# Kernel tuning notes

Hardware: AMD Instinct MI355X
Metric: run time of the kernel (lower is better)

The kernel has to match this reference:

```python
import jax, jax.numpy as jnp
import numpy as np
import math

B, S, D, H = 2, 2048, 1024, 16
DK = D // H


def setup_inputs() -> dict:
    key = jax.random.key(0)
    k1, k2, k3, k4, k5 = jax.random.split(key, 5)
    x = jax.random.normal(k1, (B, S, D), dtype=jnp.float32)
    # causal mask: True above the diagonal (positions to 'mask').
    causal_mask = jnp.triu(jnp.ones((S, S), dtype=bool), k=1)[None, None, :, :]
    scale = 1.0 / math.sqrt(D)
    W_qkv = jax.random.normal(k2, (D, 3 * D), dtype=jnp.float32) * scale
    b_qkv = jax.random.normal(k3, (3 * D,), dtype=jnp.float32) * 0.01
    W_out = jax.random.normal(k4, (D, D), dtype=jnp.float32) * scale
    b_out = jax.random.normal(k5, (D,), dtype=jnp.float32) * 0.01
    return {"x": x, "causal_mask": causal_mask, "W_qkv": W_qkv,
            "b_qkv": b_qkv, "W_out": W_out, "b_out": b_out}


def reference(x, causal_mask, W_qkv, b_qkv, W_out, b_out):
    b, s, d = x.shape
    qkv = x @ W_qkv + b_qkv                       # [b, s, 3d]
    q, k, v = jnp.split(qkv, 3, axis=-1)
    def heads(t):  # [b, s, d] -> [b, h, s, dk]
        return t.reshape(b, s, H, DK).transpose(0, 2, 1, 3)
    q, k, v = heads(q), heads(k), heads(v)
    scores = jnp.einsum("bhqd,bhkd->bhqk", q, k) / math.sqrt(DK)
    # Faithful to original: masked_fill_(mask, 1e9) uses POSITIVE 1e9.
    scores = jnp.where(causal_mask, jnp.float32(1e9), scores)
    attn = jax.nn.softmax(scores, axis=-1)        # [b, h, s, s]
    out = jnp.einsum("bhqk,bhkd->bhqd", attn, v)  # [b, h, s, dk]
    out = out.transpose(0, 2, 1, 3).reshape(b, s, d)
    return out @ W_out + b_out
```

## Files before the change

### kernel.cpp

```cpp
#include <hip/hip_runtime.h>
#include <hip/hip_bf16.h>
#include <cstdint>

constexpr int SEQ = 2048;
constexpr int DIM = 1024;
constexpr int NH = 16;
constexpr int DKH = 64;
constexpr int TRIPLE = 3072;
constexpr int BS = 2;
constexpr int MROWS = BS * SEQ;

typedef __bf16 bf16x8 __attribute__((ext_vector_type(8)));
typedef __bf16 bf16x4 __attribute__((ext_vector_type(4)));
typedef float f32x4 __attribute__((ext_vector_type(4)));

__global__ void cast_f32_bf16(const float* __restrict__ in, __bf16* __restrict__ out, int n4) {
  int i = blockIdx.x * blockDim.x + threadIdx.x;
  if (i < n4) {
    float4 v = reinterpret_cast<const float4*>(in)[i];
    bf16x4 o;
    o[0] = (__bf16)v.x; o[1] = (__bf16)v.y; o[2] = (__bf16)v.z; o[3] = (__bf16)v.w;
    reinterpret_cast<bf16x4*>(out)[i] = o;
  }
}

__global__ void transpose_cast(const float* __restrict__ W, __bf16* __restrict__ Wt,
                               int K, int N) {
  __shared__ float t[32][33];
  int c0 = blockIdx.x * 32;
  int r0 = blockIdx.y * 32;
  int tx = threadIdx.x, ty = threadIdx.y;
#pragma unroll
  for (int i = 0; i < 4; i++)
    t[ty + i * 8][tx] = W[(size_t)(r0 + ty + i * 8) * N + c0 + tx];
  __syncthreads();
#pragma unroll
  for (int i = 0; i < 4; i++)
    Wt[(size_t)(c0 + ty + i * 8) * K + r0 + tx] = (__bf16)t[tx][ty + i * 8];
}

__device__ __forceinline__ void async_copy16(const void* g, void* l) {
  __builtin_amdgcn_global_load_lds(
      (const __attribute__((address_space(1))) unsigned int*)g,
      (__attribute__((address_space(3))) unsigned int*)l, 16, 0, 0);
}

template <bool OUT_BF16>
__global__ void gemm_bt(const __bf16* __restrict__ A, const __bf16* __restrict__ Bt,
                        const float* __restrict__ bias, void* __restrict__ Cv,
                        int M, int N, int K) {
  constexpr int BM = 128, BN = 128, BK = 32;
  __shared__ __align__(16) __bf16 As[BM][BK];
  __shared__ __align__(16) __bf16 Bs[BN][BK];
  const int tid = threadIdx.x;
  const int lane = tid & 63;
  const int wave = tid >> 6;
  const int bm = blockIdx.x * BM;
  const int bn = blockIdx.y * BN;
  const int wr = (wave >> 1) * 64;
  const int wc = (wave & 1) * 64;

  f32x4 acc[4][4] = {};

  const int r15 = lane & 15;
  const int kq = (lane >> 4) * 8;

  for (int k0 = 0; k0 < K; k0 += BK) {
#pragma unroll
    for (int j = 0; j < 2; j++) {
      int seg = j * 256 + tid;
      int row = seg >> 2;
      int col = (seg & 3) * 8;
      const __bf16* ga = A + (size_t)(bm + row) * K + k0 + col;
      char* la = (char*)(&As[0][0]) + (size_t)(j * 256 + (tid & 192)) * 16;
      async_copy16(ga, la);
      const __bf16* gb = Bt + (size_t)(bn + row) * K + k0 + col;
      char* lb = (char*)(&Bs[0][0]) + (size_t)(j * 256 + (tid & 192)) * 16;
      async_copy16(gb, lb);
    }
    __syncthreads();

    bf16x8 af[4], bfr[4];
#pragma unroll
    for (int i = 0; i < 4; i++)
      af[i] = *reinterpret_cast<const bf16x8*>(&As[wr + i * 16 + r15][kq]);
#pragma unroll
    for (int j = 0; j < 4; j++)
      bfr[j] = *reinterpret_cast<const bf16x8*>(&Bs[wc + j * 16 + r15][kq]);
#pragma unroll
    for (int i = 0; i < 4; i++)
#pragma unroll
      for (int j = 0; j < 4; j++)
        acc[i][j] = __builtin_amdgcn_mfma_f32_16x16x32_bf16(af[i], bfr[j], acc[i][j], 0, 0, 0);
    __syncthreads();
  }

  __bf16* Cb = (__bf16*)Cv;
  float* Cf = (float*)Cv;
#pragma unroll
  for (int i = 0; i < 4; i++) {
    int row0 = bm + wr + i * 16 + ((lane >> 4) << 2);
#pragma unroll
    for (int j = 0; j < 4; j++) {
      int col = bn + wc + j * 16 + (lane & 15);
      float bv = bias[col];
#pragma unroll
      for (int jj = 0; jj < 4; jj++) {
        float v = acc[i][j][jj] + bv;
        if constexpr (OUT_BF16)
          Cb[(size_t)(row0 + jj) * N + col] = (__bf16)v;
        else
          Cf[(size_t)(row0 + jj) * N + col] = v;
      }
    }
  }
}

__global__ __launch_bounds__(64) void chunk_sums_k(const __bf16* __restrict__ qkv,
                                                   float* __restrict__ cs) {
  int bh = blockIdx.x, c = blockIdx.y, dk = threadIdx.x;
  int b = bh >> 4, h = bh & 15;
  const __bf16* vbase = qkv + (size_t)b * SEQ * TRIPLE + 2 * DIM + h * DKH + dk;
  float acc = 0.f;
#pragma unroll 8
  for (int kk = 0; kk < 64; kk++)
    acc += (float)vbase[(size_t)(c * 64 + kk) * TRIPLE];
  cs[((bh * 32 + c) << 6) + dk] = acc;
}

__global__ __launch_bounds__(64) void suffix_mean_k(const __bf16* __restrict__ qkv,
                                                    const float* __restrict__ cs,
                                                    __bf16* __restrict__ attn) {
  int bh = blockIdx.x, c = blockIdx.y, dk = threadIdx.x;
  int b = bh >> 4, h = bh & 15;
  float acc = 0.f;
  for (int c2 = c + 1; c2 < 32; c2++) acc += cs[((bh * 32 + c2) << 6) + dk];
  const __bf16* vbase = qkv + (size_t)b * SEQ * TRIPLE + 2 * DIM + h * DKH + dk;
  __bf16* obase = attn + (size_t)b * SEQ * DIM + h * DKH + dk;
#pragma unroll 8
  for (int kk = 63; kk >= 0; kk--) {
    int q = c * 64 + kk;
    if (q != SEQ - 1)
      obase[(size_t)q * DIM] = (__bf16)(acc / (float)(SEQ - 1 - q));
    acc += (float)vbase[(size_t)q * TRIPLE];
  }
}

__global__ __launch_bounds__(256) void last_row_attn(const __bf16* __restrict__ qkv,
                                                     __bf16* __restrict__ attn) {
  const int bh = blockIdx.x, b = bh >> 4, h = bh & 15;
  const int tid = threadIdx.x;
  __shared__ float qv[64];
  __shared__ float p[SEQ];
  __shared__ float red[4];
  __shared__ float red2[4];
  __shared__ float part[4][64];
  const __bf16* base = qkv + (size_t)b * SEQ * TRIPLE;
  if (tid < 64) qv[tid] = (float)base[(size_t)(SEQ - 1) * TRIPLE + h * DKH + tid];
  __syncthreads();
  float ls[8];
  float lmax = -1e30f;
#pragma unroll
  for (int i = 0; i < 8; i++) {
    int k = tid + i * 256;
    const bf16x8* kp = reinterpret_cast<const bf16x8*>(base + (size_t)k * TRIPLE + DIM + h * DKH);
    float dot = 0.f;
#pragma unroll
    for (int u = 0; u < 8; u++) {
      bf16x8 kv = kp[u];
#pragma unroll
      for (int e = 0; e < 8; e++) dot += qv[u * 8 + e] * (float)kv[e];
    }
    ls[i] = dot * 0.125f;
    lmax = fmaxf(lmax, ls[i]);
  }
#pragma unroll
  for (int off = 32; off >= 1; off >>= 1) lmax = fmaxf(lmax, __shfl_xor(lmax, off));
  if ((tid & 63) == 0) red[tid >> 6] = lmax;
  __syncthreads();
  lmax = fmaxf(fmaxf(red[0], red[1]), fmaxf(red[2], red[3]));
  float lsum = 0.f;
#pragma unroll
  for (int i = 0; i < 8; i++) {
    float e = expf(ls[i] - lmax);
    p[tid + i * 256] = e;
    lsum += e;
  }
#pragma unroll
  for (int off = 32; off >= 1; off >>= 1) lsum += __shfl_xor(lsum, off);
  if ((tid & 63) == 0) red2[tid >> 6] = lsum;
  __syncthreads();
  float Z = red2[0] + red2[1] + red2[2] + red2[3];
  int dk = tid & 63, ch = tid >> 6;
  float acc = 0.f;
  const __bf16* vb = base + 2 * DIM + h * DKH + dk;
  for (int k = ch * 512; k < (ch + 1) * 512; k++) acc += p[k] * (float)vb[(size_t)k * TRIPLE];
  part[ch][dk] = acc;
  __syncthreads();
  if (tid < 64) {
    float s = (part[0][tid] + part[1][tid] + part[2][tid] + part[3][tid]) / Z;
    attn[((size_t)b * SEQ + (SEQ - 1)) * DIM + h * DKH + tid] = (__bf16)s;
  }
}

extern "C" void kernel_launch(void* const* d_in, const int* in_sizes, int n_in,
                              void* d_out, int out_size, void* d_ws, size_t ws_size,
                              hipStream_t stream) {
  const float* x = (const float*)d_in[0];
  const float* Wqkv = (const float*)d_in[2];
  const float* bqkv = (const float*)d_in[3];
  const float* Wout = (const float*)d_in[4];
  const float* bout = (const float*)d_in[5];
  float* out = (float*)d_out;

  char* ws = (char*)d_ws;
  __bf16* xb = (__bf16*)ws;
  __bf16* wqkvT = (__bf16*)(ws + (8u << 20));
  __bf16* woutT = (__bf16*)(ws + (14u << 20));
  __bf16* qkvb = (__bf16*)(ws + (16u << 20));
  __bf16* attnb = (__bf16*)(ws + (40u << 20));
  float* csums = (float*)(ws + (48u << 20));

  cast_f32_bf16<<<(MROWS * DIM / 4 + 255) / 256, 256, 0, stream>>>(x, xb, MROWS * DIM / 4);
  transpose_cast<<<dim3(TRIPLE / 32, DIM / 32), dim3(32, 8), 0, stream>>>(Wqkv, wqkvT, DIM, TRIPLE);
  transpose_cast<<<dim3(DIM / 32, DIM / 32), dim3(32, 8), 0, stream>>>(Wout, woutT, DIM, DIM);

  gemm_bt<true><<<dim3(MROWS / 128, TRIPLE / 128), 256, 0, stream>>>(
      xb, wqkvT, bqkv, (void*)qkvb, MROWS, TRIPLE, DIM);

  chunk_sums_k<<<dim3(BS * NH, 32), 64, 0, stream>>>(qkvb, csums);
  suffix_mean_k<<<dim3(BS * NH, 32), 64, 0, stream>>>(qkvb, csums, attnb);
  last_row_attn<<<BS * NH, 256, 0, stream>>>(qkvb, attnb);

  gemm_bt<false><<<dim3(MROWS / 128, DIM / 128), 256, 0, stream>>>(
      attnb, woutT, bout, (void*)out, MROWS, DIM, DIM);
}
```

Measured before the change: 205.7 us.

## Skip Q projection except last row; split last-row attention across chunks

The QKV GEMM now computes only the K and V columns. The single query row still needed (the last position, the only row not fully masked) is computed by a small dot-product kernel. The last-row attention is split into 32 chunk-parallel partial softmax blocks plus a combine kernel, replacing one 256-thread block per head that ran serially over 2048 keys. This removes a third of the projection GEMM work and raises parallelism on the last-row tail, at the cost of two extra launches.

```diff
diff --git a/kernel.cpp b/kernel.cpp
--- a/kernel.cpp
+++ b/kernel.cpp
@@ -7,6 +7,7 @@
 constexpr int NH = 16;
 constexpr int DKH = 64;
 constexpr int TRIPLE = 3072;
+constexpr int KVSTR = 2048;
 constexpr int BS = 2;
 constexpr int MROWS = BS * SEQ;
 
@@ -116,91 +117,111 @@
   }
 }
 
-__global__ __launch_bounds__(64) void chunk_sums_k(const __bf16* __restrict__ qkv,
+__global__ __launch_bounds__(64) void qlast_k(const __bf16* __restrict__ xb,
+                                              const __bf16* __restrict__ wqkvT,
+                                              const float* __restrict__ bqkv,
+                                              float* __restrict__ qlast) {
+  int b = blockIdx.x;
+  int col = blockIdx.y * 64 + threadIdx.x;
+  const __bf16* xrow = xb + ((size_t)(b * SEQ + SEQ - 1)) * DIM;
+  const __bf16* wrow = wqkvT + (size_t)col * DIM;
+  float acc = 0.f;
+#pragma unroll 8
+  for (int u = 0; u < DIM / 8; u++) {
+    bf16x8 a = reinterpret_cast<const bf16x8*>(xrow)[u];
+    bf16x8 w = reinterpret_cast<const bf16x8*>(wrow)[u];
+#pragma unroll
+    for (int e = 0; e < 8; e++) acc += (float)a[e] * (float)w[e];
+  }
+  qlast[b * DIM + col] = acc + bqkv[col];
+}
+
+__global__ __launch_bounds__(64) void chunk_sums_k(const __bf16* __restrict__ kv,
                                                    float* __restrict__ cs) {
   int bh = blockIdx.x, c = blockIdx.y, dk = threadIdx.x;
   int b = bh >> 4, h = bh & 15;
-  const __bf16* vbase = qkv + (size_t)b * SEQ * TRIPLE + 2 * DIM + h * DKH + dk;
+  const __bf16* vbase = kv + (size_t)b * SEQ * KVSTR + DIM + h * DKH + dk;
   float acc = 0.f;
 #pragma unroll 8
   for (int kk = 0; kk < 64; kk++)
-    acc += (float)vbase[(size_t)(c * 64 + kk) * TRIPLE];
+    acc += (float)vbase[(size_t)(c * 64 + kk) * KVSTR];
   cs[((bh * 32 + c) << 6) + dk] = acc;
 }
 
-__global__ __launch_bounds__(64) void suffix_mean_k(const __bf16* __restrict__ qkv,
+__global__ __launch_bounds__(64) void suffix_mean_k(const __bf16* __restrict__ kv,
                                                     const float* __restrict__ cs,
                                                     __bf16* __restrict__ attn) {
   int bh = blockIdx.x, c = blockIdx.y, dk = threadIdx.x;
   int b = bh >> 4, h = bh & 15;
   float acc = 0.f;
   for (int c2 = c + 1; c2 < 32; c2++) acc += cs[((bh * 32 + c2) << 6) + dk];
-  const __bf16* vbase = qkv + (size_t)b * SEQ * TRIPLE + 2 * DIM + h * DKH + dk;
+  const __bf16* vbase = kv + (size_t)b * SEQ * KVSTR + DIM + h * DKH + dk;
   __bf16* obase = attn + (size_t)b * SEQ * DIM + h * DKH + dk;
 #pragma unroll 8
   for (int kk = 63; kk >= 0; kk--) {
     int q = c * 64 + kk;
     if (q != SEQ - 1)
       obase[(size_t)q * DIM] = (__bf16)(acc / (float)(SEQ - 1 - q));
-    acc += (float)vbase[(size_t)q * TRIPLE];
-  }
-}
-
-__global__ __launch_bounds__(256) void last_row_attn(const __bf16* __restrict__ qkv,
-                                                     __bf16* __restrict__ attn) {
+    acc += (float)vbase[(size_t)q * KVSTR];
+  }
+}
+
+__global__ __launch_bounds__(64) void lastrow_partial(const __bf16* __restrict__ kv,
+                                                      const float* __restrict__ qlast,
+                                                      float* __restrict__ pm,
+                                                      float* __restrict__ pz,
+                                                      float* __restrict__ pwv) {
+  const int bh = blockIdx.x, c = blockIdx.y;
+  const int b = bh >> 4, h = bh & 15;
+  const int t = threadIdx.x;
+  __shared__ float qs[64];
+  __shared__ float pe[64];
+  qs[t] = qlast[b * DIM + h * DKH + t];
+  __syncthreads();
+  const __bf16* krow = kv + ((size_t)(b * SEQ + c * 64 + t)) * KVSTR + h * DKH;
+  float dot = 0.f;
+#pragma unroll
+  for (int u = 0; u < 8; u++) {
+    bf16x8 kw = reinterpret_cast<const bf16x8*>(krow)[u];
+#pragma unroll
+    for (int e = 0; e < 8; e++) dot += qs[u * 8 + e] * (float)kw[e];
+  }
+  float s = dot * 0.125f;
+  float m = s;
+#pragma unroll
+  for (int off = 32; off >= 1; off >>= 1) m = fmaxf(m, __shfl_xor(m, off));
+  float e = expf(s - m);
+  float z = e;
+#pragma unroll
+  for (int off = 32; off >= 1; off >>= 1) z += __shfl_xor(z, off);
+  pe[t] = e;
+  __syncthreads();
+  const __bf16* vbase = kv + ((size_t)(b * SEQ + c * 64)) * KVSTR + DIM + h * DKH + t;
+  float acc = 0.f;
+#pragma unroll 8
+  for (int k = 0; k < 64; k++) acc += pe[k] * (float)vbase[(size_t)k * KVSTR];
+  int pi = bh * 32 + c;
+  if (t == 0) { pm[pi] = m; pz[pi] = z; }
+  pwv[pi * 64 + t] = acc;
+}
+
+__global__ __launch_bounds__(64) void lastrow_final(const float* __restrict__ pm,
+                                                    const float* __restrict__ pz,
+                                                    const float* __restrict__ pwv,
+                                                    __bf16* __restrict__ attn) {
   const int bh = blockIdx.x, b = bh >> 4, h = bh & 15;
-  const int tid = threadIdx.x;
-  __shared__ float qv[64];
-  __shared__ float p[SEQ];
-  __shared__ float red[4];
-  __shared__ float red2[4];
-  __shared__ float part[4][64];
-  const __bf16* base = qkv + (size_t)b * SEQ * TRIPLE;
-  if (tid < 64) qv[tid] = (float)base[(size_t)(SEQ - 1) * TRIPLE + h * DKH + tid];
-  __syncthreads();
-  float ls[8];
-  float lmax = -1e30f;
-#pragma unroll
-  for (int i = 0; i < 8; i++) {
-    int k = tid + i * 256;
-    const bf16x8* kp = reinterpret_cast<const bf16x8*>(base + (size_t)k * TRIPLE + DIM + h * DKH);
-    float dot = 0.f;
-#pragma unroll
-    for (int u = 0; u < 8; u++) {
-      bf16x8 kv = kp[u];
-#pragma unroll
-      for (int e = 0; e < 8; e++) dot += qv[u * 8 + e] * (float)kv[e];
-    }
-    ls[i] = dot * 0.125f;
-    lmax = fmaxf(lmax, ls[i]);
-  }
-#pragma unroll
-  for (int off = 32; off >= 1; off >>= 1) lmax = fmaxf(lmax, __shfl_xor(lmax, off));
-  if ((tid & 63) == 0) red[tid >> 6] = lmax;
-  __syncthreads();
-  lmax = fmaxf(fmaxf(red[0], red[1]), fmaxf(red[2], red[3]));
-  float lsum = 0.f;
-#pragma unroll
-  for (int i = 0; i < 8; i++) {
-    float e = expf(ls[i] - lmax);
-    p[tid + i * 256] = e;
-    lsum += e;
-  }
-#pragma unroll
-  for (int off = 32; off >= 1; off >>= 1) lsum += __shfl_xor(lsum, off);
-  if ((tid & 63) == 0) red2[tid >> 6] = lsum;
-  __syncthreads();
-  float Z = red2[0] + red2[1] + red2[2] + red2[3];
-  int dk = tid & 63, ch = tid >> 6;
-  float acc = 0.f;
-  const __bf16* vb = base + 2 * DIM + h * DKH + dk;
-  for (int k = ch * 512; k < (ch + 1) * 512; k++) acc += p[k] * (float)vb[(size_t)k * TRIPLE];
-  part[ch][dk] = acc;
-  __syncthreads();
-  if (tid < 64) {
-    float s = (part[0][tid] + part[1][tid] + part[2][tid] + part[3][tid]) / Z;
-    attn[((size_t)b * SEQ + (SEQ - 1)) * DIM + h * DKH + tid] = (__bf16)s;
-  }
+  const int t = threadIdx.x;
+  float M = -1e30f;
+#pragma unroll
+  for (int c = 0; c < 32; c++) M = fmaxf(M, pm[bh * 32 + c]);
+  float Z = 0.f, acc = 0.f;
+#pragma unroll
+  for (int c = 0; c < 32; c++) {
+    float w = expf(pm[bh * 32 + c] - M);
+    Z += pz[bh * 32 + c] * w;
+    acc += pwv[(bh * 32 + c) * 64 + t] * w;
+  }
+  attn[((size_t)b * SEQ + (SEQ - 1)) * DIM + h * DKH + t] = (__bf16)(acc / Z);
 }
 
 extern "C" void kernel_launch(void* const* d_in, const int* in_sizes, int n_in,
@@ -217,20 +238,26 @@
   __bf16* xb = (__bf16*)ws;
   __bf16* wqkvT = (__bf16*)(ws + (8u << 20));
   __bf16* woutT = (__bf16*)(ws + (14u << 20));
-  __bf16* qkvb = (__bf16*)(ws + (16u << 20));
-  __bf16* attnb = (__bf16*)(ws + (40u << 20));
-  float* csums = (float*)(ws + (48u << 20));
+  __bf16* kvb = (__bf16*)(ws + (16u << 20));
+  __bf16* attnb = (__bf16*)(ws + (32u << 20));
+  float* csums = (float*)(ws + (40u << 20));
+  float* qlast = (float*)(ws + (41u << 20));
+  float* pm = (float*)(ws + (42u << 20));
+  float* pz = (float*)(ws + (43u << 20));
+  float* pwv = (float*)(ws + (44u << 20));
 
   cast_f32_bf16<<<(MROWS * DIM / 4 + 255) / 256, 256, 0, stream>>>(x, xb, MROWS * DIM / 4);
   transpose_cast<<<dim3(TRIPLE / 32, DIM / 32), dim3(32, 8), 0, stream>>>(Wqkv, wqkvT, DIM, TRIPLE);
   transpose_cast<<<dim3(DIM / 32, DIM / 32), dim3(32, 8), 0, stream>>>(Wout, woutT, DIM, DIM);
 
-  gemm_bt<true><<<dim3(MROWS / 128, TRIPLE / 128), 256, 0, stream>>>(
-      xb, wqkvT, bqkv, (void*)qkvb, MROWS, TRIPLE, DIM);
-
-  chunk_sums_k<<<dim3(BS * NH, 32), 64, 0, stream>>>(qkvb, csums);
-  suffix_mean_k<<<dim3(BS * NH, 32), 64, 0, stream>>>(qkvb, csums, attnb);
-  last_row_attn<<<BS * NH, 256, 0, stream>>>(qkvb, attnb);
+  gemm_bt<true><<<dim3(MROWS / 128, KVSTR / 128), 256, 0, stream>>>(
+      xb, wqkvT + (size_t)DIM * DIM, bqkv + DIM, (void*)kvb, MROWS, KVSTR, DIM);
+  qlast_k<<<dim3(BS, DIM / 64), 64, 0, stream>>>(xb, wqkvT, bqkv, qlast);
+
+  chunk_sums_k<<<dim3(BS * NH, 32), 64, 0, stream>>>(kvb, csums);
+  suffix_mean_k<<<dim3(BS * NH, 32), 64, 0, stream>>>(kvb, csums, attnb);
+  lastrow_partial<<<dim3(BS * NH, 32), 64, 0, stream>>>(kvb, qlast, pm, pz, pwv);
+  lastrow_final<<<BS * NH, 64, 0, stream>>>(pm, pz, pwv, attnb);
 
   gemm_bt<false><<<dim3(MROWS / 128, DIM / 128), 256, 0, stream>>>(
       attnb, woutT, bout, (void*)out, MROWS, DIM, DIM);
```

Measured after the change: 196.3 us, median of 2. -4.6%, faster.
